# Optimization experiments

Measured on AMD Instinct MI355X. Metric: run time of the kernel, lower is better.

The kernel has to match this reference:

```python
import jax, jax.numpy as jnp
import numpy as np

B, NF, E, A = 4096, 40, 64, 32  # batch, num feature fields, embedding_size, attention_size


def setup_inputs() -> dict:
    key = jax.random.key(0)
    kx, kw, kb, kh = jax.random.split(key, 4)
    return {
        "x": jax.random.normal(kx, (B, NF, E), dtype=jnp.float32),
        "W": jax.random.normal(kw, (E, A), dtype=jnp.float32) * 0.05,  # random_normal init
        "b": jax.random.normal(kb, (A,), dtype=jnp.float32) * 0.05,
        "h": jax.random.normal(kh, (A,), dtype=jnp.float32) * 0.05,
        "p": jnp.ones((E, 1), dtype=jnp.float32),  # 'ones' initializer
    }


def reference(x, W, b, h, p):
    nf = x.shape[1]
    # pairwise (i<j) element-wise products, same ordering as the double loop
    ii, jj = np.triu_indices(nf, k=1)
    ewp = x[:, ii, :] * x[:, jj, :]                      # (B, P, E), P = nf*(nf-1)/2
    # attention MLP: relu(ewp @ W + b) . h, then exp-normalize over pairs
    a = jax.nn.relu(jnp.einsum('bpe,ea->bpa', ewp, W) + b)  # (B, P, A)
    e = jnp.exp(jnp.sum(a * h, axis=-1))                 # (B, P)  (faithful: no max-subtract)
    att = e / jnp.sum(e, axis=1, keepdims=True)          # (B, P)
    pooled = jnp.einsum('bp,bpe->be', att, ewp)          # attention-weighted sum over pairs
    return pooled @ p                                    # (B, 1)
```

## Files before the change

### kernel.cpp

```cpp
#include <hip/hip_runtime.h>

#define NFEAT 40
#define EMB   64
#define ATT   32
#define NPAIR 780
#define NPADP 784
#define NMT   49
#define XH_S  72

typedef __attribute__((ext_vector_type(8))) _Float16 f16x8;
typedef __attribute__((ext_vector_type(4))) _Float16 f16x4;
typedef __attribute__((ext_vector_type(4))) float f32x4;

template <int CTRL>
__device__ __forceinline__ float dpp_add_f(float v) {
  int t = __builtin_amdgcn_update_dpp(0, __float_as_int(v), CTRL, 0xF, 0xF, true);
  return v + __int_as_float(t);
}
__device__ __forceinline__ float rowsum16(float v) {
  v = dpp_add_f<0x128>(v);
  v = dpp_add_f<0x124>(v);
  v = dpp_add_f<0x122>(v);
  v = dpp_add_f<0x121>(v);
  return v;
}

__device__ __forceinline__ int pair_off(int i) { return 39 * i - (i * (i - 1)) / 2; }

extern "C" __global__ __launch_bounds__(256)
void afm_kernel(const float* __restrict__ xg, const float* __restrict__ Wg,
                const float* __restrict__ bg, const float* __restrict__ hg,
                const float* __restrict__ pg, float* __restrict__ outg, int nbatch) {
  __shared__ __align__(16) _Float16 xh[NFEAT * XH_S];
  __shared__ unsigned prt[NPADP];
  __shared__ float red[4][2];

  const int tid  = threadIdx.x;
  const int lane = tid & 63, wid = tid >> 6;
  const int l15  = lane & 15, hk = lane >> 4;

  for (int p = tid; p < NPADP; p += 256) {
    int i = 0, j = 0;
    if (p < NPAIR) {
      i = (int)((79.0f - sqrtf(6241.0f - 8.0f * (float)p)) * 0.5f);
      if (i < 0) i = 0;
      while (pair_off(i + 1) <= p) ++i;
      while (pair_off(i) > p) --i;
      j = i + 1 + (p - pair_off(i));
    }
    prt[p] = (unsigned)(i * 144) | ((unsigned)(j * 144) << 16);
  }

  f16x8 wf0[2], wf1[2], wf2[2];
#pragma unroll
  for (int kk = 0; kk < 2; kk++) {
    f16x8 r0, r1, r2;
#pragma unroll
    for (int t = 0; t < 8; t++) {
      int krow = kk * 32 + hk * 8 + t;
      r0[t] = (_Float16)Wg[krow * ATT + l15];
      r1[t] = (_Float16)Wg[krow * ATT + 16 + l15];
      _Float16 pv = (_Float16)pg[krow];
      r2[t] = (l15 == 0) ? pv : (_Float16)0.f;
    }
    wf0[kk] = r0; wf1[kk] = r1; wf2[kk] = r2;
  }
  const float4 b0 = *(const float4*)&bg[hk * 4];
  const float4 b1 = *(const float4*)&bg[16 + hk * 4];
  const float4 h0 = *(const float4*)&hg[hk * 4];
  const float4 h1 = *(const float4*)&hg[16 + hk * 4];

  for (int it = 0; it < 2; it++) {
    const int bb = blockIdx.x * 2 + it;
    if (bb >= nbatch) break;

    const float4* xsrc = (const float4*)(xg + (size_t)bb * (NFEAT * EMB));
    for (int f = tid; f < NFEAT * EMB / 4; f += 256) {
      float4 v = xsrc[f];
      int row = f >> 4, c = (f & 15) * 4;
      f16x4 h4 = {(_Float16)v.x, (_Float16)v.y, (_Float16)v.z, (_Float16)v.w};
      *(f16x4*)&xh[row * XH_S + c] = h4;
    }
    __syncthreads();

    float sum_e = 0.f, sum_es = 0.f;
    for (int m = wid; m < NMT; m += 4) {
      const int p0 = m * 16;
      const unsigned pij  = prt[p0 + l15];
      const unsigned offi = (pij & 0xFFFFu) + hk * 16;
      const unsigned offj = (pij >> 16) + hk * 16;
      f32x4 acc0 = {0.f, 0.f, 0.f, 0.f};
      f32x4 acc1 = {0.f, 0.f, 0.f, 0.f};
      f32x4 acc2 = {0.f, 0.f, 0.f, 0.f};
#pragma unroll
      for (int kk = 0; kk < 2; kk++) {
        const f16x8 xi = *(const f16x8*)((const char*)xh + offi + kk * 64);
        const f16x8 xj = *(const f16x8*)((const char*)xh + offj + kk * 64);
        f16x8 af = xi * xj;
        acc0 = __builtin_amdgcn_mfma_f32_16x16x32_f16(wf0[kk], af, acc0, 0, 0, 0);
        acc1 = __builtin_amdgcn_mfma_f32_16x16x32_f16(wf1[kk], af, acc1, 0, 0, 0);
        acc2 = __builtin_amdgcn_mfma_f32_16x16x32_f16(wf2[kk], af, acc2, 0, 0, 0);
      }
      float v = 0.f;
      v = fmaf(fmaxf(acc0[0] + b0.x, 0.f), h0.x, v);
      v = fmaf(fmaxf(acc0[1] + b0.y, 0.f), h0.y, v);
      v = fmaf(fmaxf(acc0[2] + b0.z, 0.f), h0.z, v);
      v = fmaf(fmaxf(acc0[3] + b0.w, 0.f), h0.w, v);
      v = fmaf(fmaxf(acc1[0] + b1.x, 0.f), h1.x, v);
      v = fmaf(fmaxf(acc1[1] + b1.y, 0.f), h1.y, v);
      v = fmaf(fmaxf(acc1[2] + b1.z, 0.f), h1.z, v);
      v = fmaf(fmaxf(acc1[3] + b1.w, 0.f), h1.w, v);
      v += __shfl_xor(v, 16, 64);
      v += __shfl_xor(v, 32, 64);
      float e = (p0 + l15 < NPAIR) ? __expf(v) : 0.f;
      sum_e += e;
      sum_es = fmaf(e, acc2[0], sum_es);
    }

    sum_e = rowsum16(sum_e);
    sum_e += __shfl_xor(sum_e, 16, 64);
    sum_e += __shfl_xor(sum_e, 32, 64);
    sum_es = rowsum16(sum_es);
    sum_es += __shfl_xor(sum_es, 16, 64);
    sum_es += __shfl_xor(sum_es, 32, 64);
    if (lane == 0) { red[wid][0] = sum_e; red[wid][1] = sum_es; }
    __syncthreads();
    if (tid == 0) {
      float Z = (red[0][0] + red[1][0] + red[2][0] + red[3][0]) * 0.25f;
      float S = red[0][1] + red[1][1] + red[2][1] + red[3][1];
      outg[bb] = S / Z;
    }
  }
}

extern "C" void kernel_launch(void* const* d_in, const int* in_sizes, int n_in,
                              void* d_out, int out_size, void* d_ws, size_t ws_size,
                              hipStream_t stream) {
  const float* xg = (const float*)d_in[0];
  const float* Wg = (const float*)d_in[1];
  const float* bg = (const float*)d_in[2];
  const float* hg = (const float*)d_in[3];
  const float* pg = (const float*)d_in[4];
  float* outg = (float*)d_out;
  const int Bn = in_sizes[0] / (NFEAT * EMB);
  const int nblk = (Bn + 1) / 2;
  afm_kernel<<<dim3(nblk), dim3(256), 0, stream>>>(xg, Wg, bg, hg, pg, outg, Bn);
}
```

Baseline: 37.60 us.

## Switch pair tiles to 32x32x16 MFMA and keep pair offsets in registers

Replaces the 16x16x32 MFMA tiling (three accumulators per 16-pair tile, 49 tiles) with 32x32x16 MFMAs over 32-pair tiles (25 tiles, two accumulators). Pair row offsets are now computed once per thread into registers, which removes the shared-memory pair table and its per-tile LDS read. Bias and h are held per accumulator row, and the normalisation factor is adjusted for the new lane duplication. The aim is fewer MFMA issues and better matrix-core efficiency. In exchange, wave 0 does seven tiles while the others do six, and register pressure rises from the 16-wide accumulators.

```diff
diff --git a/kernel.cpp b/kernel.cpp
--- a/kernel.cpp
+++ b/kernel.cpp
@@ -4,13 +4,12 @@
 #define EMB   64
 #define ATT   32
 #define NPAIR 780
-#define NPADP 784
-#define NMT   49
+#define NT    25
 #define XH_S  72
 
-typedef __attribute__((ext_vector_type(8))) _Float16 f16x8;
-typedef __attribute__((ext_vector_type(4))) _Float16 f16x4;
-typedef __attribute__((ext_vector_type(4))) float f32x4;
+typedef __attribute__((ext_vector_type(8)))  _Float16 f16x8;
+typedef __attribute__((ext_vector_type(4)))  _Float16 f16x4;
+typedef __attribute__((ext_vector_type(16))) float    f32x16;
 
 template <int CTRL>
 __device__ __forceinline__ float dpp_add_f(float v) {
@@ -32,14 +31,37 @@
                 const float* __restrict__ bg, const float* __restrict__ hg,
                 const float* __restrict__ pg, float* __restrict__ outg, int nbatch) {
   __shared__ __align__(16) _Float16 xh[NFEAT * XH_S];
-  __shared__ unsigned prt[NPADP];
   __shared__ float red[4][2];
 
   const int tid  = threadIdx.x;
   const int lane = tid & 63, wid = tid >> 6;
-  const int l15  = lane & 15, hk = lane >> 4;
+  const int l31  = lane & 31, hi = lane >> 5;
 
-  for (int p = tid; p < NPADP; p += 256) {
+  f16x8 wfA[4], pA[4];
+#pragma unroll
+  for (int kk = 0; kk < 4; kk++) {
+    f16x8 rw, rp;
+#pragma unroll
+    for (int t = 0; t < 8; t++) {
+      int krow = kk * 16 + hi * 8 + t;
+      rw[t] = (_Float16)Wg[krow * ATT + l31];
+      _Float16 pv = (_Float16)pg[krow];
+      rp[t] = (l31 == 0) ? pv : (_Float16)0.f;
+    }
+    wfA[kk] = rw; pA[kk] = rp;
+  }
+  float br[16], hr[16];
+#pragma unroll
+  for (int r = 0; r < 16; r++) {
+    int att = (r & 3) + 8 * (r >> 2) + 4 * hi;
+    br[r] = bg[att];
+    hr[r] = hg[att];
+  }
+
+  unsigned pij[7];
+#pragma unroll
+  for (int t = 0; t < 7; t++) {
+    int p = (wid + 4 * t) * 32 + l31;
     int i = 0, j = 0;
     if (p < NPAIR) {
       i = (int)((79.0f - sqrtf(6241.0f - 8.0f * (float)p)) * 0.5f);
@@ -48,27 +70,8 @@
       while (pair_off(i) > p) --i;
       j = i + 1 + (p - pair_off(i));
     }
-    prt[p] = (unsigned)(i * 144) | ((unsigned)(j * 144) << 16);
+    pij[t] = (unsigned)(i * 144 + hi * 16) | ((unsigned)(j * 144 + hi * 16) << 16);
   }
-
-  f16x8 wf0[2], wf1[2], wf2[2];
-#pragma unroll
-  for (int kk = 0; kk < 2; kk++) {
-    f16x8 r0, r1, r2;
-#pragma unroll
-    for (int t = 0; t < 8; t++) {
-      int krow = kk * 32 + hk * 8 + t;
-      r0[t] = (_Float16)Wg[krow * ATT + l15];
-      r1[t] = (_Float16)Wg[krow * ATT + 16 + l15];
-      _Float16 pv = (_Float16)pg[krow];
-      r2[t] = (l15 == 0) ? pv : (_Float16)0.f;
-    }
-    wf0[kk] = r0; wf1[kk] = r1; wf2[kk] = r2;
-  }
-  const float4 b0 = *(const float4*)&bg[hk * 4];
-  const float4 b1 = *(const float4*)&bg[16 + hk * 4];
-  const float4 h0 = *(const float4*)&hg[hk * 4];
-  const float4 h1 = *(const float4*)&hg[16 + hk * 4];
 
   for (int it = 0; it < 2; it++) {
     const int bb = blockIdx.x * 2 + it;
@@ -84,37 +87,33 @@
     __syncthreads();
 
     float sum_e = 0.f, sum_es = 0.f;
-    for (int m = wid; m < NMT; m += 4) {
-      const int p0 = m * 16;
-      const unsigned pij  = prt[p0 + l15];
-      const unsigned offi = (pij & 0xFFFFu) + hk * 16;
-      const unsigned offj = (pij >> 16) + hk * 16;
-      f32x4 acc0 = {0.f, 0.f, 0.f, 0.f};
-      f32x4 acc1 = {0.f, 0.f, 0.f, 0.f};
-      f32x4 acc2 = {0.f, 0.f, 0.f, 0.f};
 #pragma unroll
-      for (int kk = 0; kk < 2; kk++) {
-        const f16x8 xi = *(const f16x8*)((const char*)xh + offi + kk * 64);
-        const f16x8 xj = *(const f16x8*)((const char*)xh + offj + kk * 64);
-        f16x8 af = xi * xj;
-        acc0 = __builtin_amdgcn_mfma_f32_16x16x32_f16(wf0[kk], af, acc0, 0, 0, 0);
-        acc1 = __builtin_amdgcn_mfma_f32_16x16x32_f16(wf1[kk], af, acc1, 0, 0, 0);
-        acc2 = __builtin_amdgcn_mfma_f32_16x16x32_f16(wf2[kk], af, acc2, 0, 0, 0);
+    for (int t = 0; t < 7; t++) {
+      if (t < 6 || wid == 0) {
+        const unsigned offi = pij[t] & 0xFFFFu;
+        const unsigned offj = pij[t] >> 16;
+        f32x16 acc  = {0.f};
+        f32x16 acc2 = {0.f};
+#pragma unroll
+        for (int kk = 0; kk < 4; kk++) {
+          const f16x8 xi = *(const f16x8*)((const char*)xh + offi + kk * 32);
+          const f16x8 xj = *(const f16x8*)((const char*)xh + offj + kk * 32);
+          f16x8 af = xi * xj;
+          acc  = __builtin_amdgcn_mfma_f32_32x32x16_f16(wfA[kk], af, acc,  0, 0, 0);
+          acc2 = __builtin_amdgcn_mfma_f32_32x32x16_f16(pA[kk],  af, acc2, 0, 0, 0);
+        }
+        float v = 0.f;
+#pragma unroll
+        for (int r = 0; r < 16; r++)
+          v = fmaf(fmaxf(acc[r] + br[r], 0.f), hr[r], v);
+        v += __shfl_xor(v, 32, 64);
+        float s = acc2[0];
+        s += __shfl_xor(s, 32, 64);
+        int p = (wid + 4 * t) * 32 + l31;
+        float e = (p < NPAIR) ? __expf(v) : 0.f;
+        sum_e += e;
+        sum_es = fmaf(e, s, sum_es);
       }
-      float v = 0.f;
-      v = fmaf(fmaxf(acc0[0] + b0.x, 0.f), h0.x, v);
-      v = fmaf(fmaxf(acc0[1] + b0.y, 0.f), h0.y, v);
-      v = fmaf(fmaxf(acc0[2] + b0.z, 0.f), h0.z, v);
-      v = fmaf(fmaxf(acc0[3] + b0.w, 0.f), h0.w, v);
-      v = fmaf(fmaxf(acc1[0] + b1.x, 0.f), h1.x, v);
-      v = fmaf(fmaxf(acc1[1] + b1.y, 0.f), h1.y, v);
-      v = fmaf(fmaxf(acc1[2] + b1.z, 0.f), h1.z, v);
-      v = fmaf(fmaxf(acc1[3] + b1.w, 0.f), h1.w, v);
-      v += __shfl_xor(v, 16, 64);
-      v += __shfl_xor(v, 32, 64);
-      float e = (p0 + l15 < NPAIR) ? __expf(v) : 0.f;
-      sum_e += e;
-      sum_es = fmaf(e, acc2[0], sum_es);
     }
 
     sum_e = rowsum16(sum_e);
@@ -126,7 +125,7 @@
     if (lane == 0) { red[wid][0] = sum_e; red[wid][1] = sum_es; }
     __syncthreads();
     if (tid == 0) {
-      float Z = (red[0][0] + red[1][0] + red[2][0] + red[3][0]) * 0.25f;
+      float Z = red[0][0] + red[1][0] + red[2][0] + red[3][0];
       float S = red[0][1] + red[1][1] + red[2][1] + red[3][1];
       outg[bb] = S / Z;
     }
```

After: 43.33 us. +15.2%, slower.
